# Optimization experiments

Hardware: AMD Instinct MI355X
Metric: run time of the kernel (lower is better)

The kernel has to match this reference:

```python
import jax, jax.numpy as jnp
import numpy as np

DIM, D_STATE, D_CONV, EXPAND = 768, 16, 4, 2
D_INNER = EXPAND * DIM
DT_RANK = (DIM + 15) // 16  # 48
B_SZ, L_SZ = 4, 4096


def setup_inputs() -> dict:
    key = jax.random.key(0)
    ks = jax.random.split(key, 20)
    s = 0.02
    d = {}
    d['x'] = jax.random.normal(ks[0], (B_SZ, L_SZ, DIM), jnp.float32)
    d['in_proj_w'] = jax.random.normal(ks[1], (2 * D_INNER, DIM), jnp.float32) * s
    d['out_proj_w'] = jax.random.normal(ks[2], (DIM, D_INNER), jnp.float32) * s
    # forward-direction params
    d['conv1d_w'] = jax.random.normal(ks[3], (D_INNER, 1, D_CONV), jnp.float32) * s
    d['conv1d_bias'] = jax.random.normal(ks[4], (D_INNER,), jnp.float32) * s
    d['x_proj_w'] = jax.random.normal(ks[5], (DT_RANK + 2 * D_STATE, D_INNER), jnp.float32) * s
    d['dt_proj_w'] = jax.random.normal(ks[6], (D_INNER, DT_RANK), jnp.float32) * s
    d['dt_proj_bias'] = jax.random.normal(ks[7], (D_INNER,), jnp.float32) * 0.1 - 4.0
    d['A_log'] = jnp.log(jax.random.uniform(ks[8], (D_INNER, D_STATE), jnp.float32, 1.0, 16.0))
    d['D'] = jax.random.normal(ks[9], (D_INNER,), jnp.float32) * 0.1 + 1.0
    # backward-direction params (bimamba v2)
    d['conv1d_w_b'] = jax.random.normal(ks[10], (D_INNER, 1, D_CONV), jnp.float32) * s
    d['conv1d_bias_b'] = jax.random.normal(ks[11], (D_INNER,), jnp.float32) * s
    d['x_proj_w_b'] = jax.random.normal(ks[12], (DT_RANK + 2 * D_STATE, D_INNER), jnp.float32) * s
    d['dt_proj_w_b'] = jax.random.normal(ks[13], (D_INNER, DT_RANK), jnp.float32) * s
    d['dt_proj_bias_b'] = jax.random.normal(ks[14], (D_INNER,), jnp.float32) * 0.1 - 4.0
    d['A_log_b'] = jnp.log(jax.random.uniform(ks[15], (D_INNER, D_STATE), jnp.float32, 1.0, 16.0))
    d['D_b'] = jax.random.normal(ks[16], (D_INNER,), jnp.float32) * 0.1 + 1.0
    return d


def _causal_depthwise_conv(x, w, b):
    # x: (B, D, L), w: (D, 1, K) depthwise, causal left padding
    k = w.shape[-1]
    xp = jnp.pad(x, ((0, 0), (0, 0), (k - 1, 0)))
    y = jax.lax.conv_general_dilated(
        xp, w, window_strides=(1,), padding='VALID',
        dimension_numbers=('NCH', 'OIH', 'NCH'), feature_group_count=x.shape[1])
    return y + b[None, :, None]


def _selective_scan(u, dt, A, B, C, D):
    # u, dt: (b, d, l); A: (d, n); B, C: (b, n, l); D: (d,)
    b, d, l = u.shape
    n = A.shape[1]

    def step(h, inp):
        u_t, dt_t, B_t, C_t = inp  # (b,d) (b,d) (b,n) (b,n)
        dA = jnp.exp(dt_t[..., None] * A)  # (b,d,n)
        h = h * dA + dt_t[..., None] * B_t[:, None, :] * u_t[..., None]
        y = jnp.einsum('bdn,bn->bd', h, C_t)
        return h, y

    h0 = jnp.zeros((b, d, n), u.dtype)
    xs = (jnp.moveaxis(u, 2, 0), jnp.moveaxis(dt, 2, 0),
          jnp.moveaxis(B, 2, 0), jnp.moveaxis(C, 2, 0))
    _, ys = jax.lax.scan(step, h0, xs)  # ys: (l, b, d)
    y = jnp.moveaxis(ys, 0, 2)  # (b, d, l)
    return y + u * D[None, :, None]


def _one_direction(xz, conv_w, conv_b, x_proj_w, dt_w, dt_b, A_log, D):
    d_inner = xz.shape[1] // 2
    xin, z = xz[:, :d_inner], xz[:, d_inner:]  # (b,d,l) each
    xc = jax.nn.silu(_causal_depthwise_conv(xin, conv_w, conv_b))
    x_dbl = jnp.einsum('bdl,cd->bcl', xc, x_proj_w)  # (b, dt_rank+2n, l)
    dt_r = x_dbl[:, :DT_RANK]
    Bm = x_dbl[:, DT_RANK:DT_RANK + D_STATE]
    Cm = x_dbl[:, DT_RANK + D_STATE:]
    dt = jax.nn.softplus(jnp.einsum('brl,dr->bdl', dt_r, dt_w) + dt_b[None, :, None])
    A = -jnp.exp(A_log)
    y = _selective_scan(xc, dt, A, Bm, Cm, D)
    return y * jax.nn.silu(z)


def reference(x, in_proj_w, out_proj_w,
              conv1d_w, conv1d_bias, x_proj_w, dt_proj_w, dt_proj_bias, A_log, D,
              conv1d_w_b, conv1d_bias_b, x_proj_w_b, dt_proj_w_b, dt_proj_bias_b, A_log_b, D_b):
    # x: (B, L, dim)
    xz = jnp.einsum('bld,ed->bel', x, in_proj_w)  # (b, 2*d_inner, l)
    out_f = _one_direction(xz, conv1d_w, conv1d_bias, x_proj_w,
                           dt_proj_w, dt_proj_bias, A_log, D)
    out_r = _one_direction(xz[:, :, ::-1], conv1d_w_b, conv1d_bias_b, x_proj_w_b,
                           dt_proj_w_b, dt_proj_bias_b, A_log_b, D_b)
    out = out_f + out_r[:, :, ::-1]  # (b, d_inner, l)
    return jnp.einsum('bdl,od->blo', out, out_proj_w)  # (b, l, dim)
```

## Files before the change

kernel.cpp:

```cpp
#include <hip/hip_runtime.h>

#define L_SZ   4096
#define B_SZ   4
#define NCOLS  16384
#define DIM    768
#define DINNER 1536
#define E2     3072
#define DTRANK 48
#define DSTATE 16
#define NCHUNK 64
#define CLEN   64


typedef unsigned short ushortT;
typedef __attribute__((ext_vector_type(8))) short short8;
typedef __attribute__((ext_vector_type(4))) float floatx4;

__device__ __forceinline__ unsigned short f2bf(float f) {
  union { float f; unsigned u; } v; v.f = f;
  unsigned r = v.u + 0x7FFF + ((v.u >> 16) & 1);
  return (unsigned short)(r >> 16);
}
__device__ __forceinline__ float bf2f(unsigned short h) {
  union { unsigned u; float f; } v; v.u = ((unsigned)h) << 16;
  return v.f;
}

__device__ __forceinline__ float ex2(float x) {
#if defined(__has_builtin)
#if __has_builtin(__builtin_amdgcn_exp2f)
  return __builtin_amdgcn_exp2f(x);
#else
  return exp2f(x);
#endif
#else
  return exp2f(x);
#endif
}

__global__ __launch_bounds__(256) void prep_kernel(const float* __restrict__ x,
                                                   const float* __restrict__ wi,
                                                   const float* __restrict__ wo,
                                                   ushortT* __restrict__ XB,
                                                   ushortT* __restrict__ WIB,
                                                   ushortT* __restrict__ WOB,
                                                   float4* __restrict__ Z)
{
  int bid = blockIdx.x;
  if (bid < 15744) {
    const float* in; ushortT* out; int i; int n4;
    if (bid < 12288)      { in = x;  out = XB;  i = bid * 256 + threadIdx.x;            n4 = 3145728; }
    else if (bid < 14592) { in = wi; out = WIB; i = (bid - 12288) * 256 + threadIdx.x;  n4 = 589824; }
    else                  { in = wo; out = WOB; i = (bid - 14592) * 256 + threadIdx.x;  n4 = 294912; }
    if (i >= n4) return;
    float4 v = ((const float4*)in)[i];
    ushort4 o;
    o.x = f2bf(v.x); o.y = f2bf(v.y); o.z = f2bf(v.z); o.w = f2bf(v.w);
    ((ushort4*)out)[i] = o;
  } else {
    Z[(bid - 15744) * 256 + threadIdx.x] = make_float4(0.f, 0.f, 0.f, 0.f);
  }
}

__global__ __launch_bounds__(256) void zero_kernel(float4* __restrict__ p) {
  p[blockIdx.x * 256 + threadIdx.x] = make_float4(0.f, 0.f, 0.f, 0.f);
}

__global__ __launch_bounds__(256) void gemm_nt(const ushortT* __restrict__ A,
                                               const ushortT* __restrict__ Bm,
                                               float* __restrict__ Cf, ushortT* __restrict__ Cb,
                                               int M, int N, int K, int out_bf16, int G)
{
  __shared__ ushortT As[128 * 64];
  __shared__ ushortT Bs[128 * 64];
  int tid = threadIdx.x;
  int wave = tid >> 6, lane = tid & 63;
  int gid = blockIdx.y * gridDim.x + blockIdx.x;
  int per_sg = G * gridDim.y;
  int sg = gid / per_sg, r = gid % per_sg;
  int bm = r / G;
  int bn = sg * G + (r % G);
  const ushortT* Abase = A + (size_t)bm * 128 * K;
  const ushortT* Bbase = Bm + (size_t)bn * 128 * K;
  int lm = lane & 15, lq = lane >> 4;
  int wm = (wave >> 1) * 64, wn = (wave & 1) * 64;
  int rloc = lane >> 3;
  int c_st = (lane & 7) * 8;
  floatx4 acc[4][4] = {};

  for (int k0 = 0; k0 < K; k0 += 64) {
    __syncthreads();
    #pragma unroll
    for (int j = 0; j < 4; j++) {
      int t = wave * 4 + j;
      const ushortT* ga = Abase + (size_t)(t * 8 + rloc) * K + k0 + c_st;
      const ushortT* gb = Bbase + (size_t)(t * 8 + rloc) * K + k0 + c_st;
      __builtin_amdgcn_global_load_lds((const __attribute__((address_space(1))) void*)ga,
                                       (__attribute__((address_space(3))) void*)(As + t * 512),
                                       16, 0, 0);
      __builtin_amdgcn_global_load_lds((const __attribute__((address_space(1))) void*)gb,
                                       (__attribute__((address_space(3))) void*)(Bs + t * 512),
                                       16, 0, 0);
    }
    __syncthreads();
    #pragma unroll
    for (int ks = 0; ks < 2; ks++) {
      short8 af[4], bfv[4];
      #pragma unroll
      for (int i = 0; i < 4; i++)
        af[i] = *(const short8*)(As + (wm + i * 16 + lm) * 64 + ks * 32 + lq * 8);
      #pragma unroll
      for (int j2 = 0; j2 < 4; j2++)
        bfv[j2] = *(const short8*)(Bs + (wn + j2 * 16 + lm) * 64 + ks * 32 + lq * 8);
      #pragma unroll
      for (int i = 0; i < 4; i++)
        #pragma unroll
        for (int j2 = 0; j2 < 4; j2++)
          acc[i][j2] = __builtin_amdgcn_mfma_f32_16x16x32_bf16(af[i], bfv[j2], acc[i][j2], 0, 0, 0);
    }
  }
  #pragma unroll
  for (int i = 0; i < 4; i++) {
    #pragma unroll
    for (int j2 = 0; j2 < 4; j2++) {
      int mg = bm * 128 + wm + i * 16 + lq * 4;
      int ng = bn * 128 + wn + j2 * 16 + lm;
      #pragma unroll
      for (int q = 0; q < 4; q++) {
        size_t off = (size_t)(mg + q) * N + ng;
        if (out_bf16) Cb[off] = f2bf(acc[i][j2][q]);
        else          Cf[off] = acc[i][j2][q];
      }
    }
  }
}

__global__ __launch_bounds__(256) void conv_silu_kernel(const ushortT* __restrict__ xz,
                                                        const float* __restrict__ w,
                                                        const float* __restrict__ bias,
                                                        ushortT* __restrict__ xc, int reverse)
{
  int idx = blockIdx.x * 256 + threadIdx.x;
  int p4 = idx & 1023;
  int rb = idx >> 10;
  int b = rb & 3, d = rb >> 2;
  int wq = p4 >> 6, c = p4 & 63;
  int l0 = c * 64 + wq * 4;
  const ushortT* xin = xz + (size_t)d * NCOLS + b * L_SZ;
  float w0 = w[d * 4], w1 = w[d * 4 + 1], w2 = w[d * 4 + 2], w3 = w[d * 4 + 3];
  float bv = bias[d];
  float xv[8];
  float r0, r1, r2, r3;
  if (!reverse) {
    if (l0 >= 4) {
      ushort4 a = *(const ushort4*)(xin + l0 - 4);
      ushort4 cc = *(const ushort4*)(xin + l0);
      xv[0]=bf2f(a.x); xv[1]=bf2f(a.y); xv[2]=bf2f(a.z); xv[3]=bf2f(a.w);
      xv[4]=bf2f(cc.x); xv[5]=bf2f(cc.y); xv[6]=bf2f(cc.z); xv[7]=bf2f(cc.w);
    } else {
      #pragma unroll
      for (int i = 0; i < 8; i++) { int p = l0 - 4 + i; xv[i] = (p >= 0) ? bf2f(xin[p]) : 0.f; }
    }
    r0 = bv + w0*xv[1] + w1*xv[2] + w2*xv[3] + w3*xv[4];
    r1 = bv + w0*xv[2] + w1*xv[3] + w2*xv[4] + w3*xv[5];
    r2 = bv + w0*xv[3] + w1*xv[4] + w2*xv[5] + w3*xv[6];
    r3 = bv + w0*xv[4] + w1*xv[5] + w2*xv[6] + w3*xv[7];
  } else {
    int base = 4092 - l0;
    if (l0 >= 4) {
      ushort4 a = *(const ushort4*)(xin + base);
      ushort4 cc = *(const ushort4*)(xin + base + 4);
      xv[0]=bf2f(a.x); xv[1]=bf2f(a.y); xv[2]=bf2f(a.z); xv[3]=bf2f(a.w);
      xv[4]=bf2f(cc.x); xv[5]=bf2f(cc.y); xv[6]=bf2f(cc.z); xv[7]=bf2f(cc.w);
    } else {
      #pragma unroll
      for (int i = 0; i < 8; i++) { int p = base + i; xv[i] = (p <= 4095) ? bf2f(xin[p]) : 0.f; }
    }
    r0 = bv + w0*xv[6] + w1*xv[5] + w2*xv[4] + w3*xv[3];
    r1 = bv + w0*xv[5] + w1*xv[4] + w2*xv[3] + w3*xv[2];
    r2 = bv + w0*xv[4] + w1*xv[3] + w2*xv[2] + w3*xv[1];
    r3 = bv + w0*xv[3] + w1*xv[2] + w2*xv[1] + w3*xv[0];
  }
  ushort4 o;
  o.x = f2bf(r0 / (1.f + __expf(-r0)));
  o.y = f2bf(r1 / (1.f + __expf(-r1)));
  o.z = f2bf(r2 / (1.f + __expf(-r2)));
  o.w = f2bf(r3 / (1.f + __expf(-r3)));
  *(ushort4*)(xc + (size_t)d * NCOLS + b * L_SZ + p4 * 4) = o;
}

__global__ __launch_bounds__(256) void xdbl_kernel(const ushortT* __restrict__ xc,
                                                   const float* __restrict__ W,
                                                   float* __restrict__ dtr,
                                                   float* __restrict__ Bt,
                                                   float* __restrict__ Ct)
{
  __shared__ float xcs[32 * 68];
  __shared__ float Ws[80 * 32];
  int tid = threadIdx.x;
  int n0 = blockIdx.x * 64;
  int kbase = blockIdx.y * 512;
  int tm = tid >> 4, tn = tid & 15;
  float acc[5][4] = {};
  for (int k0 = kbase; k0 < kbase + 512; k0 += 32) {
    __syncthreads();
    {
      int kk = tid >> 3, c8 = (tid & 7) * 8;
      const ushortT* src = xc + (size_t)(k0 + kk) * NCOLS + n0 + c8;
      ushort4 a = *(const ushort4*)src;
      ushort4 b = *(const ushort4*)(src + 4);
      float* dst = xcs + kk * 68 + c8;
      dst[0]=bf2f(a.x); dst[1]=bf2f(a.y); dst[2]=bf2f(a.z); dst[3]=bf2f(a.w);
      dst[4]=bf2f(b.x); dst[5]=bf2f(b.y); dst[6]=bf2f(b.z); dst[7]=bf2f(b.w);
    }
    for (int i = tid; i < 80 * 32; i += 256) {
      int m = i >> 5, kk = i & 31;
      Ws[i] = W[(size_t)m * DINNER + k0 + kk];
    }
    __syncthreads();
    #pragma unroll 8
    for (int kk = 0; kk < 32; kk++) {
      const float* xr = xcs + kk * 68 + tn * 4;
      float x0 = xr[0], x1 = xr[1], x2 = xr[2], x3 = xr[3];
      #pragma unroll
      for (int im = 0; im < 5; im++) {
        float wv = Ws[(tm * 5 + im) * 32 + kk];
        acc[im][0] += wv * x0; acc[im][1] += wv * x1;
        acc[im][2] += wv * x2; acc[im][3] += wv * x3;
      }
    }
  }
  #pragma unroll
  for (int im = 0; im < 5; im++) {
    int m = tm * 5 + im;
    #pragma unroll
    for (int j = 0; j < 4; j++) {
      int n = n0 + tn * 4 + j;
      float v = acc[im][j];
      if (m < 48)      atomicAdd(&dtr[(size_t)m * NCOLS + n], v);
      else if (m < 64) atomicAdd(&Bt[(size_t)n * 16 + (m - 48)], v);
      else             atomicAdd(&Ct[(size_t)n * 16 + (m - 64)], v);
    }
  }
}

__global__ __launch_bounds__(256) void dt_kernel(const float* __restrict__ dtr,
                                                 const float* __restrict__ W,
                                                 const float* __restrict__ bias,
                                                 ushortT* __restrict__ dtb)
{
  __shared__ float sD[48 * 68];
  __shared__ float sW[48 * 68];
  int tid = threadIdx.x;
  int n0 = blockIdx.x * 64, d0 = blockIdx.y * 64;
  for (int i = tid; i < 48 * 64; i += 256) {
    int r = i >> 6, c = i & 63;
    sD[r * 68 + c] = dtr[(size_t)r * NCOLS + n0 + c];
  }
  for (int i = tid; i < 64 * 48; i += 256) {
    int dd = i / 48, k = i - dd * 48;
    sW[k * 68 + dd] = W[(size_t)d0 * 48 + i];
  }
  __syncthreads();
  int tn = tid & 15, tm = tid >> 4;
  float acc[4][4];
  #pragma unroll
  for (int i = 0; i < 4; i++) {
    float bv = bias[d0 + tm * 4 + i];
    #pragma unroll
    for (int j = 0; j < 4; j++) acc[i][j] = bv;
  }
  #pragma unroll 6
  for (int k = 0; k < 48; k++) {
    float4 wv = *(const float4*)(sW + k * 68 + tm * 4);
    float4 xv = *(const float4*)(sD + k * 68 + tn * 4);
    float wa[4] = { wv.x, wv.y, wv.z, wv.w };
    float xa[4] = { xv.x, xv.y, xv.z, xv.w };
    #pragma unroll
    for (int i = 0; i < 4; i++)
      #pragma unroll
      for (int j = 0; j < 4; j++)
        acc[i][j] += wa[i] * xa[j];
  }
  #pragma unroll
  for (int i = 0; i < 4; i++) {
    int d = d0 + tm * 4 + i;
    ushort4 o;
    float a0 = acc[i][0], a1 = acc[i][1], a2 = acc[i][2], a3 = acc[i][3];
    o.x = f2bf((a0 > 20.f) ? a0 : log1pf(__expf(a0)));
    o.y = f2bf((a1 > 20.f) ? a1 : log1pf(__expf(a1)));
    o.z = f2bf((a2 > 20.f) ? a2 : log1pf(__expf(a2)));
    o.w = f2bf((a3 > 20.f) ? a3 : log1pf(__expf(a3)));
    *(ushort4*)(dtb + (size_t)d * NCOLS + n0 + tn * 4) = o;
  }
}

__global__ __launch_bounds__(256) void scan_kernel12(const ushortT* __restrict__ u,
                                                     const ushortT* __restrict__ dt,
                                                     const float* __restrict__ Bt,
                                                     const float* __restrict__ Ct,
                                                     const float* __restrict__ A_log,
                                                     const float* __restrict__ Dp,
                                                     ushortT* __restrict__ y, int reverse)
{
  __shared__ float Hs[32 * 65];
  __shared__ float Ss[2 * 64];
  __shared__ float Y1s[2 * 4096];
  int tid = threadIdx.x;
  int hf = tid & 1;
  int c  = (tid >> 1) & 63;
  int dl = tid >> 7;
  int b = blockIdx.y;
  int d = blockIdx.x * 2 + dl;
  int ns0 = hf * 8;

  float Av2[8];
  #pragma unroll
  for (int n = 0; n < 8; n++)
    Av2[n] = -__expf(A_log[d * 16 + ns0 + n]) * 1.442695040888963f;
  float Dv = Dp[d];

  const ushortT* ur = u + (size_t)d * NCOLS + b * L_SZ + c * 4;
  const ushortT* tr = dt + (size_t)d * NCOLS + b * L_SZ + c * 4;
  const float*   Bp = Bt + (size_t)b * L_SZ * 16 + ns0;
  const float*   Cp = Ct + (size_t)b * L_SZ * 16 + ns0;

  float h[8];
  float S = 0.f;
  #pragma unroll
  for (int n = 0; n < 8; n++) h[n] = 0.f;

  ushort4 uA = *(const ushort4*)(ur);
  ushort4 tA = *(const ushort4*)(tr);
  ushort4 uB = *(const ushort4*)(ur + 256);
  ushort4 tB = *(const ushort4*)(tr + 256);
  #pragma unroll 2
  for (int w = 0; w < 16; w++) {
    int wn2 = (w + 2) & 15;
    ushort4 uC = *(const ushort4*)(ur + wn2 * 256);
    ushort4 tC = *(const ushort4*)(tr + wn2 * 256);
    float uv[4] = { bf2f(uA.x), bf2f(uA.y), bf2f(uA.z), bf2f(uA.w) };
    float tv[4] = { bf2f(tA.x), bf2f(tA.y), bf2f(tA.z), bf2f(tA.w) };
    const float* Bw = Bp + (size_t)(w * 256 + c * 4) * 16;
    const float* Cw = Cp + (size_t)(w * 256 + c * 4) * 16;
    float yo[4];
    #pragma unroll
    for (int q = 0; q < 4; q++) {
      float tq = tv[q];
      float dtu = tq * uv[q];
      float4 b0 = *(const float4*)(Bw + q * 16);
      float4 b1 = *(const float4*)(Bw + q * 16 + 4);
      float4 c0 = *(const float4*)(Cw + q * 16);
      float4 c1 = *(const float4*)(Cw + q * 16 + 4);
      float Bf[8] = { b0.x,b0.y,b0.z,b0.w, b1.x,b1.y,b1.z,b1.w };
      float Cv[8] = { c0.x,c0.y,c0.z,c0.w, c1.x,c1.y,c1.z,c1.w };
      float a0 = 0.f, a1 = 0.f;
      #pragma unroll
      for (int n = 0; n < 4; n++) {
        float e = ex2(tq * Av2[n]);
        h[n] = h[n] * e + Bf[n] * dtu;
        a0 += h[n] * Cv[n];
      }
      #pragma unroll
      for (int n = 4; n < 8; n++) {
        float e = ex2(tq * Av2[n]);
        h[n] = h[n] * e + Bf[n] * dtu;
        a1 += h[n] * Cv[n];
      }
      yo[q] = a0 + a1;
      S += tq;
    }
    float os0 = __shfl_xor(yo[0], 1);
    float os1 = __shfl_xor(yo[1], 1);
    float os2 = __shfl_xor(yo[2], 1);
    float os3 = __shfl_xor(yo[3], 1);
    if (hf == 0) {
      float4 yq;
      yq.x = yo[0] + os0 + Dv * uv[0];
      yq.y = yo[1] + os1 + Dv * uv[1];
      yq.z = yo[2] + os2 + Dv * uv[2];
      yq.w = yo[3] + os3 + Dv * uv[3];
      *(float4*)(Y1s + dl * 4096 + w * 256 + c * 4) = yq;
    }
    uA = uB; tA = tB; uB = uC; tB = tC;
  }
  #pragma unroll
  for (int n = 0; n < 8; n++)
    Hs[(dl * 16 + ns0 + n) * 65 + c] = h[n];
  if (hf == 0) Ss[dl * 64 + c] = S;
  __syncthreads();

  if (tid < 32) {
    int dl2 = tid >> 4, n2 = tid & 15;
    float Ac = -__expf(A_log[(blockIdx.x * 2 + dl2) * 16 + n2]) * 1.442695040888963f;
    float hsv = 0.f;
    int row = tid;
    for (int cc = 0; cc < NCHUNK; cc++) {
      int idx = row * 65 + cc;
      float tmp = Hs[idx];
      Hs[idx] = hsv;
      hsv = ex2(Ac * Ss[dl2 * 64 + cc]) * hsv + tmp;
    }
  }
  __syncthreads();
  float hsr[8];
  #pragma unroll
  for (int n = 0; n < 8; n++) hsr[n] = Hs[(dl * 16 + ns0 + n) * 65 + c];

  ushortT* yrow = y + (size_t)d * NCOLS + b * L_SZ;
  float T = 0.f;
  #pragma unroll 2
  for (int w = 0; w < 16; w++) {
    ushort4 t4b = *(const ushort4*)(tr + w * 256);
    float tv[4]  = { bf2f(t4b.x), bf2f(t4b.y), bf2f(t4b.z), bf2f(t4b.w) };
    float4 y1q = *(const float4*)(Y1s + dl * 4096 + w * 256 + c * 4);
    const float* Cw = Cp + (size_t)(w * 256 + c * 4) * 16;
    float co[4];
    #pragma unroll
    for (int q = 0; q < 4; q++) {
      T += tv[q];
      float4 c0 = *(const float4*)(Cw + q * 16);
      float4 c1 = *(const float4*)(Cw + q * 16 + 4);
      float Cv[8] = { c0.x,c0.y,c0.z,c0.w, c1.x,c1.y,c1.z,c1.w };
      float a0 = 0.f, a1 = 0.f;
      #pragma unroll
      for (int n = 0; n < 4; n++)
        a0 += (ex2(Av2[n] * T) * hsr[n]) * Cv[n];
      #pragma unroll
      for (int n = 4; n < 8; n++)
        a1 += (ex2(Av2[n] * T) * hsr[n]) * Cv[n];
      co[q] = a0 + a1;
    }
    float os0 = __shfl_xor(co[0], 1);
    float os1 = __shfl_xor(co[1], 1);
    float os2 = __shfl_xor(co[2], 1);
    float os3 = __shfl_xor(co[3], 1);
    if (hf == 0) {
      float yq0 = y1q.x + co[0] + os0;
      float yq1 = y1q.y + co[1] + os1;
      float yq2 = y1q.z + co[2] + os2;
      float yq3 = y1q.w + co[3] + os3;
      if (!reverse) {
        ushort4 o;
        o.x = f2bf(yq0); o.y = f2bf(yq1); o.z = f2bf(yq2); o.w = f2bf(yq3);
        *(ushort4*)(yrow + w * 256 + c * 4) = o;
      } else {
        ushort4* dst = (ushort4*)(yrow + (15 - w) * 256 + (63 - c) * 4);
        ushort4 old = *dst;
        ushort4 o;
        o.x = f2bf(bf2f(old.x) + yq3);
        o.y = f2bf(bf2f(old.y) + yq2);
        o.z = f2bf(bf2f(old.z) + yq1);
        o.w = f2bf(bf2f(old.w) + yq0);
        *dst = o;
      }
    }
  }
}

__global__ __launch_bounds__(256) void inner_kernel(const ushortT* __restrict__ y,
                                                    const ushortT* __restrict__ xz,
                                                    ushortT* __restrict__ innerb)
{
  __shared__ float tile[64 * 65];
  int n0 = blockIdx.x * 64, d0 = blockIdx.y * 64;
  int tid = threadIdx.x;
  int c = tid & 63, rq = tid >> 6;
  int bseg = n0 & ~4095;
  int cch = (n0 & 4095) >> 6;
  int poff = bseg + cch * 4 + (c >> 2) * 256 + (c & 3);
  #pragma unroll
  for (int r = 0; r < 16; r++) {
    int dd = rq + r * 4;
    float yv = bf2f(y[(size_t)(d0 + dd) * NCOLS + poff]);
    float zv = bf2f(xz[(size_t)(DINNER + d0 + dd) * NCOLS + n0 + c]);
    float sv = zv / (1.f + __expf(-zv));
    tile[dd * 65 + c] = yv * sv;
  }
  __syncthreads();
  #pragma unroll
  for (int r = 0; r < 16; r++) {
    int nn = rq + r * 4;
    innerb[(size_t)(n0 + nn) * DINNER + d0 + c] = f2bf(tile[c * 65 + nn]);
  }
}

extern "C" void kernel_launch(void* const* d_in, const int* in_sizes, int n_in,
                              void* d_out, int out_size, void* d_ws, size_t ws_size,
                              hipStream_t stream)
{
  const float* x          = (const float*)d_in[0];
  const float* in_proj_w  = (const float*)d_in[1];
  const float* out_proj_w = (const float*)d_in[2];
  const float* conv_w     = (const float*)d_in[3];
  const float* conv_b     = (const float*)d_in[4];
  const float* xproj_w    = (const float*)d_in[5];
  const float* dt_w       = (const float*)d_in[6];
  const float* dt_b       = (const float*)d_in[7];
  const float* A_log      = (const float*)d_in[8];
  const float* Dp         = (const float*)d_in[9];
  const float* conv_w_b   = (const float*)d_in[10];
  const float* conv_b_b   = (const float*)d_in[11];
  const float* xproj_w_b  = (const float*)d_in[12];
  const float* dt_w_b     = (const float*)d_in[13];
  const float* dt_b_b     = (const float*)d_in[14];
  const float* A_log_b    = (const float*)d_in[15];
  const float* D_b        = (const float*)d_in[16];

  char* ws = (char*)d_ws;
  ushortT* XZ   = (ushortT*)(ws + 0);
  ushortT* XC   = (ushortT*)(ws + 100663296);
  ushortT* YB   = (ushortT*)(ws + 150994944);
  float*   DTR  = (float*)  (ws + 201326592);
  float*   BT   = (float*)  (ws + 204472320);
  float*   CT   = (float*)  (ws + 205520896);
  ushortT* WOB  = (ushortT*)(ws + 206569472);
  ushortT* XB   = (ushortT*)(ws + 100663296);
  ushortT* WIB  = (ushortT*)(ws + 150994944);
  ushortT* DTB  = (ushortT*)d_out;
  ushortT* INNER = XZ;
  float* OUT = (float*)d_out;

  prep_kernel<<<17024, 256, 0, stream>>>(x, in_proj_w, out_proj_w, XB, WIB, WOB, (float4*)DTR);

  gemm_nt<<<dim3(128, 24), 256, 0, stream>>>(WIB, XB, nullptr, XZ, E2, NCOLS, DIM, 1, 16);

  conv_silu_kernel<<<24576, 256, 0, stream>>>(XZ, conv_w, conv_b, XC, 0);
  xdbl_kernel<<<dim3(256, 3), 256, 0, stream>>>(XC, xproj_w, DTR, BT, CT);
  dt_kernel<<<dim3(256, 24), 256, 0, stream>>>(DTR, dt_w, dt_b, DTB);
  scan_kernel12<<<dim3(768, 4), 256, 0, stream>>>(XC, DTB, BT, CT, A_log, Dp, YB, 0);

  conv_silu_kernel<<<24576, 256, 0, stream>>>(XZ, conv_w_b, conv_b_b, XC, 1);
  zero_kernel<<<1280, 256, 0, stream>>>((float4*)DTR);
  xdbl_kernel<<<dim3(256, 3), 256, 0, stream>>>(XC, xproj_w_b, DTR, BT, CT);
  dt_kernel<<<dim3(256, 24), 256, 0, stream>>>(DTR, dt_w_b, dt_b_b, DTB);
  scan_kernel12<<<dim3(768, 4), 256, 0, stream>>>(XC, DTB, BT, CT, A_log_b, D_b, YB, 1);

  inner_kernel<<<dim3(256, 24), 256, 0, stream>>>(YB, XZ, INNER);

  gemm_nt<<<dim3(6, 128), 256, 0, stream>>>(INNER, WOB, OUT, nullptr, NCOLS, DIM, DINNER, 0, 6);
}
```

Baseline: 1.632 ms.

## Split scan into 128 chunks of 32 with one channel per block

Changes the chunked selective scan from 64 chunks of 64 steps (two channels per block) to 128 chunks of 32 steps with one channel per block. The conv, scan and inner kernels' interleaved column layout is updated to match. This shortens the serial per-thread recurrence and doubles the grid, meant to expose more parallelism and latency hiding. In exchange, the serial cross-chunk pass done by 16 threads is twice as long, and the chunk-offset correction costs more per element.

```diff
diff --git a/kernel.cpp b/kernel.cpp
--- a/kernel.cpp
+++ b/kernel.cpp
@@ -8,8 +8,8 @@
 #define E2     3072
 #define DTRANK 48
 #define DSTATE 16
-#define NCHUNK 64
-#define CLEN   64
+#define NCHUNK 128
+#define CLEN   32
 
 
 typedef unsigned short ushortT;
@@ -144,8 +144,8 @@
   int p4 = idx & 1023;
   int rb = idx >> 10;
   int b = rb & 3, d = rb >> 2;
-  int wq = p4 >> 6, c = p4 & 63;
-  int l0 = c * 64 + wq * 4;
+  int wq = p4 >> 7, c = p4 & 127;
+  int l0 = c * 32 + wq * 4;
   const ushortT* xin = xz + (size_t)d * NCOLS + b * L_SZ;
   float w0 = w[d * 4], w1 = w[d * 4 + 1], w2 = w[d * 4 + 2], w3 = w[d * 4 + 3];
   float bv = bias[d];
@@ -295,7 +295,7 @@
   }
 }
 
-__global__ __launch_bounds__(256) void scan_kernel12(const ushortT* __restrict__ u,
+__global__ __launch_bounds__(256) void scan_kernel14(const ushortT* __restrict__ u,
                                                      const ushortT* __restrict__ dt,
                                                      const float* __restrict__ Bt,
                                                      const float* __restrict__ Ct,
@@ -303,15 +303,14 @@
                                                      const float* __restrict__ Dp,
                                                      ushortT* __restrict__ y, int reverse)
 {
-  __shared__ float Hs[32 * 65];
-  __shared__ float Ss[2 * 64];
-  __shared__ float Y1s[2 * 4096];
+  __shared__ float Hs[16 * 129];
+  __shared__ float Ss[128];
+  __shared__ float Y1s[4096];
   int tid = threadIdx.x;
   int hf = tid & 1;
-  int c  = (tid >> 1) & 63;
-  int dl = tid >> 7;
+  int c  = tid >> 1;
   int b = blockIdx.y;
-  int d = blockIdx.x * 2 + dl;
+  int d = blockIdx.x;
   int ns0 = hf * 8;
 
   float Av2[8];
@@ -332,17 +331,16 @@
 
   ushort4 uA = *(const ushort4*)(ur);
   ushort4 tA = *(const ushort4*)(tr);
-  ushort4 uB = *(const ushort4*)(ur + 256);
-  ushort4 tB = *(const ushort4*)(tr + 256);
-  #pragma unroll 2
-  for (int w = 0; w < 16; w++) {
-    int wn2 = (w + 2) & 15;
-    ushort4 uC = *(const ushort4*)(ur + wn2 * 256);
-    ushort4 tC = *(const ushort4*)(tr + wn2 * 256);
+  ushort4 uB = *(const ushort4*)(ur + 512);
+  ushort4 tB = *(const ushort4*)(tr + 512);
+  for (int w = 0; w < 8; w++) {
+    int wn2 = (w + 2) & 7;
+    ushort4 uC = *(const ushort4*)(ur + wn2 * 512);
+    ushort4 tC = *(const ushort4*)(tr + wn2 * 512);
     float uv[4] = { bf2f(uA.x), bf2f(uA.y), bf2f(uA.z), bf2f(uA.w) };
     float tv[4] = { bf2f(tA.x), bf2f(tA.y), bf2f(tA.z), bf2f(tA.w) };
-    const float* Bw = Bp + (size_t)(w * 256 + c * 4) * 16;
-    const float* Cw = Cp + (size_t)(w * 256 + c * 4) * 16;
+    const float* Bw = Bp + (size_t)(w * 512 + c * 4) * 16;
+    const float* Cw = Cp + (size_t)(w * 512 + c * 4) * 16;
     float yo[4];
     #pragma unroll
     for (int q = 0; q < 4; q++) {
@@ -380,41 +378,39 @@
       yq.y = yo[1] + os1 + Dv * uv[1];
       yq.z = yo[2] + os2 + Dv * uv[2];
       yq.w = yo[3] + os3 + Dv * uv[3];
-      *(float4*)(Y1s + dl * 4096 + w * 256 + c * 4) = yq;
+      *(float4*)(Y1s + w * 512 + c * 4) = yq;
     }
     uA = uB; tA = tB; uB = uC; tB = tC;
   }
   #pragma unroll
   for (int n = 0; n < 8; n++)
-    Hs[(dl * 16 + ns0 + n) * 65 + c] = h[n];
-  if (hf == 0) Ss[dl * 64 + c] = S;
+    Hs[(ns0 + n) * 129 + c] = h[n];
+  if (hf == 0) Ss[c] = S;
   __syncthreads();
 
-  if (tid < 32) {
-    int dl2 = tid >> 4, n2 = tid & 15;
-    float Ac = -__expf(A_log[(blockIdx.x * 2 + dl2) * 16 + n2]) * 1.442695040888963f;
+  if (tid < 16) {
+    float Ac = -__expf(A_log[d * 16 + tid]) * 1.442695040888963f;
     float hsv = 0.f;
-    int row = tid;
     for (int cc = 0; cc < NCHUNK; cc++) {
-      int idx = row * 65 + cc;
+      int idx = tid * 129 + cc;
       float tmp = Hs[idx];
       Hs[idx] = hsv;
-      hsv = ex2(Ac * Ss[dl2 * 64 + cc]) * hsv + tmp;
+      hsv = ex2(Ac * Ss[cc]) * hsv + tmp;
     }
   }
   __syncthreads();
   float hsr[8];
   #pragma unroll
-  for (int n = 0; n < 8; n++) hsr[n] = Hs[(dl * 16 + ns0 + n) * 65 + c];
+  for (int n = 0; n < 8; n++) hsr[n] = Hs[(ns0 + n) * 129 + c];
 
   ushortT* yrow = y + (size_t)d * NCOLS + b * L_SZ;
   float T = 0.f;
   #pragma unroll 2
-  for (int w = 0; w < 16; w++) {
-    ushort4 t4b = *(const ushort4*)(tr + w * 256);
+  for (int w = 0; w < 8; w++) {
+    ushort4 t4b = *(const ushort4*)(tr + w * 512);
     float tv[4]  = { bf2f(t4b.x), bf2f(t4b.y), bf2f(t4b.z), bf2f(t4b.w) };
-    float4 y1q = *(const float4*)(Y1s + dl * 4096 + w * 256 + c * 4);
-    const float* Cw = Cp + (size_t)(w * 256 + c * 4) * 16;
+    float4 y1q = *(const float4*)(Y1s + w * 512 + c * 4);
+    const float* Cw = Cp + (size_t)(w * 512 + c * 4) * 16;
     float co[4];
     #pragma unroll
     for (int q = 0; q < 4; q++) {
@@ -443,9 +439,9 @@
       if (!reverse) {
         ushort4 o;
         o.x = f2bf(yq0); o.y = f2bf(yq1); o.z = f2bf(yq2); o.w = f2bf(yq3);
-        *(ushort4*)(yrow + w * 256 + c * 4) = o;
+        *(ushort4*)(yrow + w * 512 + c * 4) = o;
       } else {
-        ushort4* dst = (ushort4*)(yrow + (15 - w) * 256 + (63 - c) * 4);
+        ushort4* dst = (ushort4*)(yrow + (7 - w) * 512 + (127 - c) * 4);
         ushort4 old = *dst;
         ushort4 o;
         o.x = f2bf(bf2f(old.x) + yq3);
@@ -467,8 +463,8 @@
   int tid = threadIdx.x;
   int c = tid & 63, rq = tid >> 6;
   int bseg = n0 & ~4095;
-  int cch = (n0 & 4095) >> 6;
-  int poff = bseg + cch * 4 + (c >> 2) * 256 + (c & 3);
+  int pl = (n0 & 4095) + c;
+  int poff = bseg + ((pl & 31) >> 2) * 512 + (pl >> 5) * 4 + (pl & 3);
   #pragma unroll
   for (int r = 0; r < 16; r++) {
     int dd = rq + r * 4;
@@ -528,13 +524,13 @@
   conv_silu_kernel<<<24576, 256, 0, stream>>>(XZ, conv_w, conv_b, XC, 0);
   xdbl_kernel<<<dim3(256, 3), 256, 0, stream>>>(XC, xproj_w, DTR, BT, CT);
   dt_kernel<<<dim3(256, 24), 256, 0, stream>>>(DTR, dt_w, dt_b, DTB);
-  scan_kernel12<<<dim3(768, 4), 256, 0, stream>>>(XC, DTB, BT, CT, A_log, Dp, YB, 0);
+  scan_kernel14<<<dim3(1536, 4), 256, 0, stream>>>(XC, DTB, BT, CT, A_log, Dp, YB, 0);
 
   conv_silu_kernel<<<24576, 256, 0, stream>>>(XZ, conv_w_b, conv_b_b, XC, 1);
   zero_kernel<<<1280, 256, 0, stream>>>((float4*)DTR);
   xdbl_kernel<<<dim3(256, 3), 256, 0, stream>>>(XC, xproj_w_b, DTR, BT, CT);
   dt_kernel<<<dim3(256, 24), 256, 0, stream>>>(DTR, dt_w_b, dt_b_b, DTB);
-  scan_kernel12<<<dim3(768, 4), 256, 0, stream>>>(XC, DTB, BT, CT, A_log_b, D_b, YB, 1);
+  scan_kernel14<<<dim3(1536, 4), 256, 0, stream>>>(XC, DTB, BT, CT, A_log_b, D_b, YB, 1);
 
   inner_kernel<<<dim3(256, 24), 256, 0, stream>>>(YB, XZ, INNER);
 
```

Measured after the change: 1.653 ms. No clear change (+1.3%).
